# Kernel optimization log

Hardware: AMD Instinct MI355X
Metric: run time of the kernel (lower is better)

Reference implementation:

```python
import jax, jax.numpy as jnp
import numpy as np

BS, NF, MAXC, NLOC = 8, 32, 4, 65536
DELTA_VAR, DELTA_DIST = 0.5, 1.5
ALPHA, BETA, GAMMA = 1.0, 1.0, 1e-4
K_ACTIVE = 2  # every sample has exactly 2 active clusters (indices 0,1), matching the
              # original code's len(class_index)==2 filter in _cluster_means


def _safe_norm(sq):
    # sqrt of sum-of-squares with a zero-safe gradient (torch.norm subgradient at 0 is 0)
    s = jnp.where(sq > 0, sq, 1.0)
    return jnp.where(sq > 0, jnp.sqrt(s), 0.0)


def setup_inputs() -> dict:
    key = jax.random.key(0)
    k1, k2 = jax.random.split(key)
    inp = jax.random.normal(k1, (BS, NF, NLOC), dtype=jnp.float32)
    labels = jax.random.randint(k2, (BS, NLOC), 0, K_ACTIVE)  # only clusters 0,1 populated
    target = jnp.transpose(jax.nn.one_hot(labels, MAXC, dtype=jnp.float32), (0, 2, 1))  # (BS, MAXC, NLOC)
    n_clusters = jnp.full((BS,), K_ACTIVE, dtype=jnp.int32)
    return {"input": inp, "target": target, "n_clusters": n_clusters}


def reference(input, target, n_clusters):
    nc = n_clusters.astype(jnp.float32)                      # (bs,)
    counts = target.sum(-1)                                  # (bs, maxc) pixels per cluster
    active = counts > 0
    safe_counts = jnp.where(active, counts, 1.0)

    # cluster means: masked segment-mean, zeros for padded/inactive clusters
    sums = jnp.einsum('bfn,bcn->bfc', input, target)          # (bs, nf, maxc)
    means = jnp.where(active[:, None, :], sums / safe_counts[:, None, :], 0.0)

    # variance term: pull embeddings within delta_var of their cluster mean
    diff = input[:, :, None, :] - means[:, :, :, None]        # (bs, nf, maxc, nloc)
    dist = _safe_norm(jnp.sum(diff * diff, axis=1))           # (bs, maxc, nloc) L2 over features
    var = jnp.maximum(dist - DELTA_VAR, 0.0) ** 2 * target
    c_var = jnp.where(active, var.sum(-1) / safe_counts, 0.0)  # per-cluster mean
    l_var = jnp.mean(c_var.sum(-1) / nc)

    # distance term: push cluster means at least 2*delta_dist apart (K_ACTIVE clusters)
    m = means[:, :, :K_ACTIVE]                                # (bs, nf, K)
    d = m[:, :, :, None] - m[:, :, None, :]                   # (bs, nf, K, K)
    dn = _safe_norm(jnp.sum(d * d, axis=1))                   # (bs, K, K)
    margin = 2.0 * DELTA_DIST * (1.0 - jnp.eye(K_ACTIVE, dtype=jnp.float32))
    c_dist = jnp.sum(jnp.maximum(margin - dn, 0.0) ** 2, axis=(1, 2))
    l_dist = jnp.mean(c_dist / (2.0 * nc * (nc - 1.0)))

    # regularization: mean L2 norm of the active cluster means
    l_reg = jnp.mean(jnp.mean(_safe_norm(jnp.sum(m * m, axis=1)), axis=-1))

    return ALPHA * l_var + BETA * l_dist + GAMMA * l_reg
```

## Files before the change

kernel.cpp:

```cpp
#include <hip/hip_runtime.h>
#include <math.h>

#define BS 8
#define NF 32
#define NLOC 65536
#define DELTA_VAR 0.5f
#define DELTA_DIST 1.5f
#define GAMMA 1e-4f
#define G 128
#define CHUNK 512
#define G2 64
#define CHUNK2 1024

#define WS_COUNTS 0
#define WS_MEANS  16
#define WS_VARSUM 528
#define WS_PART   1040
#define WS_LABELS (1040 + BS * G * 68)

__global__ __launch_bounds__(256, 4) void k_sums(const float* __restrict__ inp,
                                                 const float* __restrict__ tgt,
                                                 float* __restrict__ ws,
                                                 unsigned char* __restrict__ labels) {
  float* part = ws + WS_PART;
  const int b = blockIdx.y;
  const int gx = blockIdx.x;
  const int tid = threadIdx.x;
  const int lane = tid & 63;
  const int fg = tid >> 6;
  const int n0 = gx * CHUNK;
  const float* inp_b = inp + (size_t)b * NF * NLOC + (size_t)fg * 8 * NLOC;
  const float* t0_b = tgt + (size_t)b * 4 * NLOC;

  float r[16];
#pragma unroll
  for (int k = 0; k < 16; ++k) r[k] = 0.f;
  float cnt0 = 0.f;

#pragma unroll
  for (int it = 0; it < CHUNK / 256; ++it) {
    const int n = n0 + it * 256 + lane * 4;
    float4 t0 = *reinterpret_cast<const float4*>(t0_b + n);
    float4 x[8];
#pragma unroll
    for (int i = 0; i < 8; ++i)
      x[i] = *reinterpret_cast<const float4*>(inp_b + i * NLOC + n);
    if (fg == 0) {
      cnt0 += t0.x + t0.y + t0.z + t0.w;
      uchar4 l4;
      l4.x = t0.x > 0.5f ? 0 : 1;
      l4.y = t0.y > 0.5f ? 0 : 1;
      l4.z = t0.z > 0.5f ? 0 : 1;
      l4.w = t0.w > 0.5f ? 0 : 1;
      *reinterpret_cast<uchar4*>(labels + (size_t)b * NLOC + n) = l4;
    }
#pragma unroll
    for (int i = 0; i < 8; ++i) {
      r[i * 2 + 0] += x[i].x + x[i].y + x[i].z + x[i].w;
      r[i * 2 + 1] += x[i].x * t0.x + x[i].y * t0.y + x[i].z * t0.z + x[i].w * t0.w;
    }
  }

#define BSTEP(m, half)                                      \
  {                                                         \
    _Pragma("unroll") for (int j = 0; j < half; ++j) {      \
      float aa = __shfl_xor(r[j], m, 64);                   \
      float bb = __shfl_xor(r[j + half], m, 64);            \
      r[j] = (lane & m) ? (r[j + half] + bb) : (r[j] + aa); \
    }                                                       \
  }
  BSTEP(32, 8)
  BSTEP(16, 4)
  BSTEP(8, 2)
  BSTEP(4, 1)
#undef BSTEP
  r[0] += __shfl_xor(r[0], 2, 64);
  r[0] += __shfl_xor(r[0], 1, 64);

  __shared__ float pp[68];
  if ((lane & 3) == 0) pp[fg * 16 + (lane >> 2)] = r[0];

  if (fg == 0) {
    cnt0 += __shfl_xor(cnt0, 32, 64);
    cnt0 += __shfl_xor(cnt0, 16, 64);
    cnt0 += __shfl_xor(cnt0, 8, 64);
    cnt0 += __shfl_xor(cnt0, 4, 64);
    cnt0 += __shfl_xor(cnt0, 2, 64);
    cnt0 += __shfl_xor(cnt0, 1, 64);
    if (lane == 0) pp[64] = cnt0;
  }
  __syncthreads();
  if (tid < 65) part[((size_t)(b * G + gx)) * 68 + tid] = pp[tid];
  if (gx == 0 && tid < 2) ws[WS_VARSUM + (b * 2 + tid) * 32] = 0.f;
}

__global__ __launch_bounds__(256, 4) void k_var(const float* __restrict__ inp,
                                                const unsigned char* __restrict__ labels,
                                                float* __restrict__ ws) {
  const int b = blockIdx.y;
  const int gx = blockIdx.x;
  const int tid = threadIdx.x;
  const int lane = tid & 63;
  const int fg = tid >> 6;

  __shared__ float sbuf[4][64];
  __shared__ float tbuf[64];
  __shared__ float cbuf[G];
  __shared__ float cnt_s[2];
  __shared__ float2 m_lds[NF];
  __shared__ float vred[4][2];

  {
    const float* pb = ws + WS_PART + (size_t)b * G * 68;
    const int q = tid >> 6, rem = tid & 63;
    float s = 0.f;
    for (int g2 = q * 32; g2 < q * 32 + 32; ++g2) s += pb[(size_t)g2 * 68 + rem];
    sbuf[q][rem] = s;
    if (tid < G) cbuf[tid] = pb[(size_t)tid * 68 + 64];
    __syncthreads();
    if (tid < 64) {
      tbuf[tid] = sbuf[0][tid] + sbuf[1][tid] + sbuf[2][tid] + sbuf[3][tid];
      float c = cbuf[tid] + cbuf[tid + 64];
      c += __shfl_xor(c, 32, 64);
      c += __shfl_xor(c, 16, 64);
      c += __shfl_xor(c, 8, 64);
      c += __shfl_xor(c, 4, 64);
      c += __shfl_xor(c, 2, 64);
      c += __shfl_xor(c, 1, 64);
      if (tid == 0) {
        cnt_s[0] = c;
        cnt_s[1] = (float)NLOC - c;
      }
    }
    __syncthreads();
    if (tid < 32) {
      const int f = tid;
      float sx = tbuf[f * 2], s0 = tbuf[f * 2 + 1];
      float c0 = cnt_s[0], c1 = cnt_s[1];
      float m0 = c0 > 0.f ? s0 / c0 : 0.f;
      float m1 = c1 > 0.f ? (sx - s0) / c1 : 0.f;
      m_lds[f] = make_float2(m0, m1);
      if (gx == 0) {
        ws[WS_MEANS + (b * NF + f) * 2 + 0] = m0;
        ws[WS_MEANS + (b * NF + f) * 2 + 1] = m1;
        if (f < 2) ws[WS_COUNTS + b * 2 + f] = cnt_s[f];
      }
    }
    __syncthreads();
  }

  {
    const float* inp_b = inp + (size_t)b * NF * NLOC;
    const int n = gx * CHUNK2 + tid * 4;
    const uchar4 lab = *reinterpret_cast<const uchar4*>(labels + (size_t)b * NLOC + n);
    float a0 = 0.f, a1 = 0.f, a2 = 0.f, a3 = 0.f;
#pragma unroll
    for (int f = 0; f < NF; ++f) {
      float4 x = *reinterpret_cast<const float4*>(inp_b + f * NLOC + n);
      float2 m = m_lds[f];
      float m0 = lab.x ? m.y : m.x;
      float m1 = lab.y ? m.y : m.x;
      float m2 = lab.z ? m.y : m.x;
      float m3 = lab.w ? m.y : m.x;
      float d0 = x.x - m0, d1 = x.y - m1, d2 = x.z - m2, d3 = x.w - m3;
      a0 += d0 * d0;
      a1 += d1 * d1;
      a2 += d2 * d2;
      a3 += d3 * d3;
    }
    float v0 = fmaxf(sqrtf(a0) - DELTA_VAR, 0.f);
    float v1 = fmaxf(sqrtf(a1) - DELTA_VAR, 0.f);
    float v2 = fmaxf(sqrtf(a2) - DELTA_VAR, 0.f);
    float v3 = fmaxf(sqrtf(a3) - DELTA_VAR, 0.f);
    v0 *= v0; v1 *= v1; v2 *= v2; v3 *= v3;
    float vacc0 = (lab.x ? 0.f : v0) + (lab.y ? 0.f : v1) +
                  (lab.z ? 0.f : v2) + (lab.w ? 0.f : v3);
    float vacc1 = (lab.x ? v0 : 0.f) + (lab.y ? v1 : 0.f) +
                  (lab.z ? v2 : 0.f) + (lab.w ? v3 : 0.f);

    float aa = __shfl_xor(vacc0, 32, 64);
    float bb = __shfl_xor(vacc1, 32, 64);
    float u = (lane & 32) ? (vacc1 + bb) : (vacc0 + aa);
    u += __shfl_xor(u, 16, 64);
    u += __shfl_xor(u, 8, 64);
    u += __shfl_xor(u, 4, 64);
    u += __shfl_xor(u, 2, 64);
    u += __shfl_xor(u, 1, 64);
    if ((lane & 31) == 0) vred[fg][lane >> 5] = u;
    __syncthreads();
    if (tid < 2) {
      float s = vred[0][tid] + vred[1][tid] + vred[2][tid] + vred[3][tid];
      atomicAdd(&ws[WS_VARSUM + (b * 2 + tid) * 32], s);
    }
  }
}

__global__ void k_final(const float* __restrict__ ws,
                        const int* __restrict__ ncl,
                        float* __restrict__ out) {
  const int tid = threadIdx.x;
  float total = 0.f;
  if (tid < BS) {
    const int b = tid;
    const float nc = (float)ncl[b];
    float c0 = ws[WS_COUNTS + b * 2 + 0], c1 = ws[WS_COUNTS + b * 2 + 1];
    float v0 = ws[WS_VARSUM + (b * 2 + 0) * 32], v1 = ws[WS_VARSUM + (b * 2 + 1) * 32];
    float sv = (c0 > 0.f ? v0 / c0 : 0.f) + (c1 > 0.f ? v1 / c1 : 0.f);
    float l_var = sv / nc;
    float d2 = 0.f, n0s = 0.f, n1s = 0.f;
    for (int f = 0; f < NF; ++f) {
      float m0 = ws[WS_MEANS + (b * NF + f) * 2 + 0];
      float m1 = ws[WS_MEANS + (b * NF + f) * 2 + 1];
      float df = m0 - m1;
      d2 += df * df;
      n0s += m0 * m0;
      n1s += m1 * m1;
    }
    float dn = d2 > 0.f ? sqrtf(d2) : 0.f;
    float h = fmaxf(2.f * DELTA_DIST - dn, 0.f);
    float l_dist = 2.f * h * h / (2.f * nc * (nc - 1.f));
    float r0 = n0s > 0.f ? sqrtf(n0s) : 0.f;
    float r1 = n1s > 0.f ? sqrtf(n1s) : 0.f;
    float l_reg = 0.5f * (r0 + r1);
    total = l_var + l_dist + GAMMA * l_reg;
  }
#pragma unroll
  for (int m = 1; m < 8; m <<= 1) total += __shfl_xor(total, m, 64);
  if (tid == 0) out[0] = total / (float)BS;
}

extern "C" void kernel_launch(void* const* d_in, const int* in_sizes, int n_in,
                              void* d_out, int out_size, void* d_ws, size_t ws_size,
                              hipStream_t stream) {
  const float* inp = (const float*)d_in[0];
  const float* tgt = (const float*)d_in[1];
  const int* ncl = (const int*)d_in[2];
  float* out = (float*)d_out;
  float* ws = (float*)d_ws;
  unsigned char* labels = (unsigned char*)(ws + WS_LABELS);

  k_sums<<<dim3(G, BS), 256, 0, stream>>>(inp, tgt, ws, labels);
  k_var<<<dim3(G2, BS), 256, 0, stream>>>(inp, labels, ws);
  k_final<<<1, 64, 0, stream>>>(ws, ncl, out);
}
```

Baseline: 34.06 us.

## Reduce cluster sums per (feature,batch) block to drop partials and k_var reduction

k_sums now launches one 1024-thread block per (feature, batch) that reduces an entire 65536-long row, writing final sums and counts directly. This removes the per-chunk partial buffer and the prologue in every k_var block that re-reduced 128 partials. k_final recomputes means from sums. The cost is that each block re-reads the target row, and the grid is smaller (256 large blocks instead of 1024), which may lower memory-level parallelism.

```diff
diff --git a/kernel.cpp b/kernel.cpp
--- a/kernel.cpp
+++ b/kernel.cpp
@@ -7,91 +7,77 @@
 #define DELTA_VAR 0.5f
 #define DELTA_DIST 1.5f
 #define GAMMA 1e-4f
-#define G 128
-#define CHUNK 512
 #define G2 64
 #define CHUNK2 1024
 
-#define WS_COUNTS 0
-#define WS_MEANS  16
+#define WS_CNT0   0
+#define WS_SUMS   16
 #define WS_VARSUM 528
-#define WS_PART   1040
-#define WS_LABELS (1040 + BS * G * 68)
-
-__global__ __launch_bounds__(256, 4) void k_sums(const float* __restrict__ inp,
-                                                 const float* __restrict__ tgt,
-                                                 float* __restrict__ ws,
-                                                 unsigned char* __restrict__ labels) {
-  float* part = ws + WS_PART;
+#define WS_LABELS 1040
+
+__global__ __launch_bounds__(1024) void k_sums(const float* __restrict__ inp,
+                                               const float* __restrict__ tgt,
+                                               float* __restrict__ ws,
+                                               unsigned char* __restrict__ labels) {
+  const int f = blockIdx.x;
   const int b = blockIdx.y;
-  const int gx = blockIdx.x;
   const int tid = threadIdx.x;
   const int lane = tid & 63;
-  const int fg = tid >> 6;
-  const int n0 = gx * CHUNK;
-  const float* inp_b = inp + (size_t)b * NF * NLOC + (size_t)fg * 8 * NLOC;
-  const float* t0_b = tgt + (size_t)b * 4 * NLOC;
-
-  float r[16];
-#pragma unroll
-  for (int k = 0; k < 16; ++k) r[k] = 0.f;
-  float cnt0 = 0.f;
-
-#pragma unroll
-  for (int it = 0; it < CHUNK / 256; ++it) {
-    const int n = n0 + it * 256 + lane * 4;
-    float4 t0 = *reinterpret_cast<const float4*>(t0_b + n);
-    float4 x[8];
-#pragma unroll
-    for (int i = 0; i < 8; ++i)
-      x[i] = *reinterpret_cast<const float4*>(inp_b + i * NLOC + n);
-    if (fg == 0) {
-      cnt0 += t0.x + t0.y + t0.z + t0.w;
-      uchar4 l4;
-      l4.x = t0.x > 0.5f ? 0 : 1;
-      l4.y = t0.y > 0.5f ? 0 : 1;
-      l4.z = t0.z > 0.5f ? 0 : 1;
-      l4.w = t0.w > 0.5f ? 0 : 1;
-      *reinterpret_cast<uchar4*>(labels + (size_t)b * NLOC + n) = l4;
+  const int wave = tid >> 6;
+  const float* row = inp + ((size_t)b * NF + f) * NLOC;
+  const float* trow = tgt + (size_t)b * 4 * NLOC;
+
+  float sx = 0.f, s0 = 0.f, cnt = 0.f;
+#pragma unroll
+  for (int it = 0; it < NLOC / 4096; ++it) {
+    const int n = it * 4096 + tid * 4;
+    float4 x = *reinterpret_cast<const float4*>(row + n);
+    float4 t = *reinterpret_cast<const float4*>(trow + n);
+    sx += x.x + x.y + x.z + x.w;
+    s0 += x.x * t.x + x.y * t.y + x.z * t.z + x.w * t.w;
+    if (f == 0) cnt += t.x + t.y + t.z + t.w;
+  }
+
+  if (tid < 512) {
+    const int n = f * 2048 + tid * 4;
+    float4 t = *reinterpret_cast<const float4*>(trow + n);
+    uchar4 l4;
+    l4.x = t.x > 0.5f ? 0 : 1;
+    l4.y = t.y > 0.5f ? 0 : 1;
+    l4.z = t.z > 0.5f ? 0 : 1;
+    l4.w = t.w > 0.5f ? 0 : 1;
+    *reinterpret_cast<uchar4*>(labels + (size_t)b * NLOC + n) = l4;
+  }
+
+  __shared__ float red[16][3];
+#pragma unroll
+  for (int m = 32; m >= 1; m >>= 1) {
+    sx += __shfl_xor(sx, m, 64);
+    s0 += __shfl_xor(s0, m, 64);
+  }
+  if (f == 0) {
+#pragma unroll
+    for (int m = 32; m >= 1; m >>= 1) cnt += __shfl_xor(cnt, m, 64);
+  }
+  if (lane == 0) {
+    red[wave][0] = sx;
+    red[wave][1] = s0;
+    red[wave][2] = cnt;
+  }
+  __syncthreads();
+  if (tid == 0) {
+    float SX = 0.f, S0 = 0.f, C = 0.f;
+#pragma unroll
+    for (int w = 0; w < 16; ++w) {
+      SX += red[w][0];
+      S0 += red[w][1];
+      C += red[w][2];
     }
-#pragma unroll
-    for (int i = 0; i < 8; ++i) {
-      r[i * 2 + 0] += x[i].x + x[i].y + x[i].z + x[i].w;
-      r[i * 2 + 1] += x[i].x * t0.x + x[i].y * t0.y + x[i].z * t0.z + x[i].w * t0.w;
-    }
-  }
-
-#define BSTEP(m, half)                                      \
-  {                                                         \
-    _Pragma("unroll") for (int j = 0; j < half; ++j) {      \
-      float aa = __shfl_xor(r[j], m, 64);                   \
-      float bb = __shfl_xor(r[j + half], m, 64);            \
-      r[j] = (lane & m) ? (r[j + half] + bb) : (r[j] + aa); \
-    }                                                       \
-  }
-  BSTEP(32, 8)
-  BSTEP(16, 4)
-  BSTEP(8, 2)
-  BSTEP(4, 1)
-#undef BSTEP
-  r[0] += __shfl_xor(r[0], 2, 64);
-  r[0] += __shfl_xor(r[0], 1, 64);
-
-  __shared__ float pp[68];
-  if ((lane & 3) == 0) pp[fg * 16 + (lane >> 2)] = r[0];
-
-  if (fg == 0) {
-    cnt0 += __shfl_xor(cnt0, 32, 64);
-    cnt0 += __shfl_xor(cnt0, 16, 64);
-    cnt0 += __shfl_xor(cnt0, 8, 64);
-    cnt0 += __shfl_xor(cnt0, 4, 64);
-    cnt0 += __shfl_xor(cnt0, 2, 64);
-    cnt0 += __shfl_xor(cnt0, 1, 64);
-    if (lane == 0) pp[64] = cnt0;
-  }
-  __syncthreads();
-  if (tid < 65) part[((size_t)(b * G + gx)) * 68 + tid] = pp[tid];
-  if (gx == 0 && tid < 2) ws[WS_VARSUM + (b * 2 + tid) * 32] = 0.f;
+    ws[WS_SUMS + ((size_t)b * NF + f) * 2 + 0] = SX;
+    ws[WS_SUMS + ((size_t)b * NF + f) * 2 + 1] = S0;
+    if (f == 0) ws[WS_CNT0 + b] = C;
+  }
+  if (f == 0 && tid < 2) ws[WS_VARSUM + (b * 2 + tid) * 32] = 0.f;
 }
 
 __global__ __launch_bounds__(256, 4) void k_var(const float* __restrict__ inp,
@@ -103,95 +89,61 @@
   const int lane = tid & 63;
   const int fg = tid >> 6;
 
-  __shared__ float sbuf[4][64];
-  __shared__ float tbuf[64];
-  __shared__ float cbuf[G];
-  __shared__ float cnt_s[2];
   __shared__ float2 m_lds[NF];
   __shared__ float vred[4][2];
 
-  {
-    const float* pb = ws + WS_PART + (size_t)b * G * 68;
-    const int q = tid >> 6, rem = tid & 63;
-    float s = 0.f;
-    for (int g2 = q * 32; g2 < q * 32 + 32; ++g2) s += pb[(size_t)g2 * 68 + rem];
-    sbuf[q][rem] = s;
-    if (tid < G) cbuf[tid] = pb[(size_t)tid * 68 + 64];
-    __syncthreads();
-    if (tid < 64) {
-      tbuf[tid] = sbuf[0][tid] + sbuf[1][tid] + sbuf[2][tid] + sbuf[3][tid];
-      float c = cbuf[tid] + cbuf[tid + 64];
-      c += __shfl_xor(c, 32, 64);
-      c += __shfl_xor(c, 16, 64);
-      c += __shfl_xor(c, 8, 64);
-      c += __shfl_xor(c, 4, 64);
-      c += __shfl_xor(c, 2, 64);
-      c += __shfl_xor(c, 1, 64);
-      if (tid == 0) {
-        cnt_s[0] = c;
-        cnt_s[1] = (float)NLOC - c;
-      }
-    }
-    __syncthreads();
-    if (tid < 32) {
-      const int f = tid;
-      float sx = tbuf[f * 2], s0 = tbuf[f * 2 + 1];
-      float c0 = cnt_s[0], c1 = cnt_s[1];
-      float m0 = c0 > 0.f ? s0 / c0 : 0.f;
-      float m1 = c1 > 0.f ? (sx - s0) / c1 : 0.f;
-      m_lds[f] = make_float2(m0, m1);
-      if (gx == 0) {
-        ws[WS_MEANS + (b * NF + f) * 2 + 0] = m0;
-        ws[WS_MEANS + (b * NF + f) * 2 + 1] = m1;
-        if (f < 2) ws[WS_COUNTS + b * 2 + f] = cnt_s[f];
-      }
-    }
-    __syncthreads();
-  }
-
-  {
-    const float* inp_b = inp + (size_t)b * NF * NLOC;
-    const int n = gx * CHUNK2 + tid * 4;
-    const uchar4 lab = *reinterpret_cast<const uchar4*>(labels + (size_t)b * NLOC + n);
-    float a0 = 0.f, a1 = 0.f, a2 = 0.f, a3 = 0.f;
-#pragma unroll
-    for (int f = 0; f < NF; ++f) {
-      float4 x = *reinterpret_cast<const float4*>(inp_b + f * NLOC + n);
-      float2 m = m_lds[f];
-      float m0 = lab.x ? m.y : m.x;
-      float m1 = lab.y ? m.y : m.x;
-      float m2 = lab.z ? m.y : m.x;
-      float m3 = lab.w ? m.y : m.x;
-      float d0 = x.x - m0, d1 = x.y - m1, d2 = x.z - m2, d3 = x.w - m3;
-      a0 += d0 * d0;
-      a1 += d1 * d1;
-      a2 += d2 * d2;
-      a3 += d3 * d3;
-    }
-    float v0 = fmaxf(sqrtf(a0) - DELTA_VAR, 0.f);
-    float v1 = fmaxf(sqrtf(a1) - DELTA_VAR, 0.f);
-    float v2 = fmaxf(sqrtf(a2) - DELTA_VAR, 0.f);
-    float v3 = fmaxf(sqrtf(a3) - DELTA_VAR, 0.f);
-    v0 *= v0; v1 *= v1; v2 *= v2; v3 *= v3;
-    float vacc0 = (lab.x ? 0.f : v0) + (lab.y ? 0.f : v1) +
-                  (lab.z ? 0.f : v2) + (lab.w ? 0.f : v3);
-    float vacc1 = (lab.x ? v0 : 0.f) + (lab.y ? v1 : 0.f) +
-                  (lab.z ? v2 : 0.f) + (lab.w ? v3 : 0.f);
-
-    float aa = __shfl_xor(vacc0, 32, 64);
-    float bb = __shfl_xor(vacc1, 32, 64);
-    float u = (lane & 32) ? (vacc1 + bb) : (vacc0 + aa);
-    u += __shfl_xor(u, 16, 64);
-    u += __shfl_xor(u, 8, 64);
-    u += __shfl_xor(u, 4, 64);
-    u += __shfl_xor(u, 2, 64);
-    u += __shfl_xor(u, 1, 64);
-    if ((lane & 31) == 0) vred[fg][lane >> 5] = u;
-    __syncthreads();
-    if (tid < 2) {
-      float s = vred[0][tid] + vred[1][tid] + vred[2][tid] + vred[3][tid];
-      atomicAdd(&ws[WS_VARSUM + (b * 2 + tid) * 32], s);
-    }
+  if (tid < 32) {
+    const float c0 = ws[WS_CNT0 + b];
+    const float c1 = (float)NLOC - c0;
+    const float sx = ws[WS_SUMS + ((size_t)b * NF + tid) * 2 + 0];
+    const float s0 = ws[WS_SUMS + ((size_t)b * NF + tid) * 2 + 1];
+    const float m0 = c0 > 0.f ? s0 / c0 : 0.f;
+    const float m1 = c1 > 0.f ? (sx - s0) / c1 : 0.f;
+    m_lds[tid] = make_float2(m0, m1);
+  }
+  __syncthreads();
+
+  const float* inp_b = inp + (size_t)b * NF * NLOC;
+  const int n = gx * CHUNK2 + tid * 4;
+  const uchar4 lab = *reinterpret_cast<const uchar4*>(labels + (size_t)b * NLOC + n);
+  float a0 = 0.f, a1 = 0.f, a2 = 0.f, a3 = 0.f;
+#pragma unroll
+  for (int f = 0; f < NF; ++f) {
+    float4 x = *reinterpret_cast<const float4*>(inp_b + f * NLOC + n);
+    float2 m = m_lds[f];
+    float m0 = lab.x ? m.y : m.x;
+    float m1 = lab.y ? m.y : m.x;
+    float m2 = lab.z ? m.y : m.x;
+    float m3 = lab.w ? m.y : m.x;
+    float d0 = x.x - m0, d1 = x.y - m1, d2 = x.z - m2, d3 = x.w - m3;
+    a0 += d0 * d0;
+    a1 += d1 * d1;
+    a2 += d2 * d2;
+    a3 += d3 * d3;
+  }
+  float v0 = fmaxf(sqrtf(a0) - DELTA_VAR, 0.f);
+  float v1 = fmaxf(sqrtf(a1) - DELTA_VAR, 0.f);
+  float v2 = fmaxf(sqrtf(a2) - DELTA_VAR, 0.f);
+  float v3 = fmaxf(sqrtf(a3) - DELTA_VAR, 0.f);
+  v0 *= v0; v1 *= v1; v2 *= v2; v3 *= v3;
+  float vacc0 = (lab.x ? 0.f : v0) + (lab.y ? 0.f : v1) +
+                (lab.z ? 0.f : v2) + (lab.w ? 0.f : v3);
+  float vacc1 = (lab.x ? v0 : 0.f) + (lab.y ? v1 : 0.f) +
+                (lab.z ? v2 : 0.f) + (lab.w ? v3 : 0.f);
+
+  float aa = __shfl_xor(vacc0, 32, 64);
+  float bb = __shfl_xor(vacc1, 32, 64);
+  float u = (lane & 32) ? (vacc1 + bb) : (vacc0 + aa);
+  u += __shfl_xor(u, 16, 64);
+  u += __shfl_xor(u, 8, 64);
+  u += __shfl_xor(u, 4, 64);
+  u += __shfl_xor(u, 2, 64);
+  u += __shfl_xor(u, 1, 64);
+  if ((lane & 31) == 0) vred[fg][lane >> 5] = u;
+  __syncthreads();
+  if (tid < 2) {
+    float s = vred[0][tid] + vred[1][tid] + vred[2][tid] + vred[3][tid];
+    atomicAdd(&ws[WS_VARSUM + (b * 2 + tid) * 32], s);
   }
 }
 
@@ -203,14 +155,18 @@
   if (tid < BS) {
     const int b = tid;
     const float nc = (float)ncl[b];
-    float c0 = ws[WS_COUNTS + b * 2 + 0], c1 = ws[WS_COUNTS + b * 2 + 1];
-    float v0 = ws[WS_VARSUM + (b * 2 + 0) * 32], v1 = ws[WS_VARSUM + (b * 2 + 1) * 32];
+    const float c0 = ws[WS_CNT0 + b];
+    const float c1 = (float)NLOC - c0;
+    float v0 = ws[WS_VARSUM + (b * 2 + 0) * 32];
+    float v1 = ws[WS_VARSUM + (b * 2 + 1) * 32];
     float sv = (c0 > 0.f ? v0 / c0 : 0.f) + (c1 > 0.f ? v1 / c1 : 0.f);
     float l_var = sv / nc;
     float d2 = 0.f, n0s = 0.f, n1s = 0.f;
     for (int f = 0; f < NF; ++f) {
-      float m0 = ws[WS_MEANS + (b * NF + f) * 2 + 0];
-      float m1 = ws[WS_MEANS + (b * NF + f) * 2 + 1];
+      float sx = ws[WS_SUMS + ((size_t)b * NF + f) * 2 + 0];
+      float s0 = ws[WS_SUMS + ((size_t)b * NF + f) * 2 + 1];
+      float m0 = c0 > 0.f ? s0 / c0 : 0.f;
+      float m1 = c1 > 0.f ? (sx - s0) / c1 : 0.f;
       float df = m0 - m1;
       d2 += df * df;
       n0s += m0 * m0;
@@ -239,7 +195,7 @@
   float* ws = (float*)d_ws;
   unsigned char* labels = (unsigned char*)(ws + WS_LABELS);
 
-  k_sums<<<dim3(G, BS), 256, 0, stream>>>(inp, tgt, ws, labels);
+  k_sums<<<dim3(NF, BS), 1024, 0, stream>>>(inp, tgt, ws, labels);
   k_var<<<dim3(G2, BS), 256, 0, stream>>>(inp, labels, ws);
   k_final<<<1, 64, 0, stream>>>(ws, ncl, out);
 }
```

Measured after the change: 46.60 us. +36.8%, slower.
